# Kernel tuning notes

Measured on AMD Instinct MI355X. Metric: run time of the kernel, lower is better.

The kernel has to match this reference:

```python
import jax, jax.numpy as jnp
import numpy as np

DIM = 1024
HEADS = 16
DIM_HEAD = 64
INNER = HEADS * DIM_HEAD  # 1024
SCALE = DIM ** (-0.5)     # NOTE: source uses dim, not dim_head, for scaling


def setup_inputs() -> dict:
    key = jax.random.key(0)
    k_x, k_qkv, k_out = jax.random.split(key, 3)
    x = jax.random.normal(k_x, (4, 2048, DIM), dtype=jnp.float32)
    # store weights pre-transposed: y = x @ W  (equivalent to torch Linear with W.T)
    w_qkv = jax.random.normal(k_qkv, (DIM, 3 * INNER), dtype=jnp.float32) * 0.02
    w_out = jax.random.normal(k_out, (INNER, DIM), dtype=jnp.float32) * 0.02
    b_out = jnp.zeros((DIM,), dtype=jnp.float32)
    return {"x": x, "w_qkv": w_qkv, "w_out": w_out, "b_out": b_out}


def reference(x, w_qkv, w_out, b_out):
    b, n, _ = x.shape
    qkv = x @ w_qkv                                  # [b, n, 3*inner]
    q, k, v = jnp.split(qkv, 3, axis=-1)             # each [b, n, inner]

    def to_heads(t):
        return t.reshape(b, n, HEADS, DIM_HEAD).transpose(0, 2, 1, 3)  # [b, h, n, d]

    q, k, v = to_heads(q), to_heads(k), to_heads(v)
    dots = jnp.einsum("bhid,bhjd->bhij", q, k) * SCALE   # [b, h, n, n]
    attn = jax.nn.softmax(dots, axis=-1)
    out = jnp.einsum("bhij,bhjd->bhid", attn, v)         # [b, h, n, d]
    out = out.transpose(0, 2, 1, 3).reshape(b, n, INNER)  # [b, n, inner]
    return out @ w_out + b_out                            # dropout p=0 -> identity
```

## Files before the change

kernel.cpp:

```cpp
#include <hip/hip_runtime.h>
#include <math.h>

#define BATCH   4
#define NSEQ    2048
#define DIM     1024
#define HEADS   16
#define DHEAD   64
#define INNER   1024
#define MTOT    (BATCH*NSEQ)
#define SC_L2E  0.04508422f

typedef __attribute__((ext_vector_type(8))) unsigned short u16x8;
typedef __attribute__((ext_vector_type(4))) unsigned short u16x4;
typedef __attribute__((ext_vector_type(8))) short          bf16x8;
typedef __attribute__((ext_vector_type(4))) float          f32x4;

__device__ __forceinline__ unsigned short f2bf(float f) {
    unsigned int u = __builtin_bit_cast(unsigned int, f);
    u += 0x7FFFu + ((u >> 16) & 1u);
    return (unsigned short)(u >> 16);
}

__device__ __forceinline__ float fexp2(float x) {
    float r; asm("v_exp_f32 %0, %1" : "=v"(r) : "v"(x)); return r;
}

__device__ __forceinline__ unsigned int cvtpk(float lo, float hi) {
    unsigned int r; asm("v_cvt_pk_bf16_f32 %0, %1, %2" : "=v"(r) : "v"(lo), "v"(hi));
    return r;
}

#define GLDS16(gp, lp) __builtin_amdgcn_global_load_lds( \
    (const __attribute__((address_space(1))) unsigned int*)(gp), \
    (__attribute__((address_space(3))) unsigned int*)(lp), 16, 0, 0)

#define SWC(r, c) ((c) ^ (((r) & 7) << 3))

__global__ __launch_bounds__(256) void cvt_bf16(const float* __restrict__ in,
                                                unsigned short* __restrict__ out)
{
    const int i = blockIdx.x * 256 + threadIdx.x;
    const float4* p = reinterpret_cast<const float4*>(in) + (size_t)i * 2;
    float4 a = p[0], b = p[1];
    u16x8 o;
    o[0]=f2bf(a.x); o[1]=f2bf(a.y); o[2]=f2bf(a.z); o[3]=f2bf(a.w);
    o[4]=f2bf(b.x); o[5]=f2bf(b.y); o[6]=f2bf(b.z); o[7]=f2bf(b.w);
    reinterpret_cast<u16x8*>(out)[i] = o;
}

__global__ __launch_bounds__(256) void transp_bf16(const float* __restrict__ in,
                                                   unsigned short* __restrict__ out,
                                                   int R, int C)
{
    __shared__ float tile[32][33];
    const int c0 = blockIdx.x * 32, r0 = blockIdx.y * 32;
    const int tx = threadIdx.x & 31, ty = threadIdx.x >> 5;
#pragma unroll
    for (int i = 0; i < 32; i += 8)
        tile[ty + i][tx] = in[(size_t)(r0 + ty + i) * C + c0 + tx];
    __syncthreads();
#pragma unroll
    for (int i = 0; i < 32; i += 8)
        out[(size_t)(c0 + ty + i) * R + r0 + tx] = f2bf(tile[tx][ty + i]);
}


__global__ __launch_bounds__(256) void gemm_qkv_mfma(const unsigned short* __restrict__ A,
                                                     const unsigned short* __restrict__ Bt,
                                                     unsigned short* __restrict__ qb,
                                                     unsigned short* __restrict__ kb,
                                                     unsigned short* __restrict__ vt)
{
    __shared__ unsigned short As[128][32];
    __shared__ unsigned short Bs[128][32];

    const int t = threadIdx.x;
    const int l = t & 63, w = t >> 6;
    const int wr = w >> 1, wc = w & 1;
    const int g = l >> 4, ql = l & 15;

    const int lin  = blockIdx.x + 24 * blockIdx.y;
    const int nlin = (lin & 7) * 192 + (lin >> 3);
    const int bx = nlin % 24, by = nlin / 24;
    const int row0 = by * 128;
    const int col0 = bx * 128;
    const int lr = l >> 2, lc = l & 3;

    f32x4 acc[4][4];
#pragma unroll
    for (int mi = 0; mi < 4; ++mi)
#pragma unroll
        for (int ni = 0; ni < 4; ++ni)
#pragma unroll
            for (int r = 0; r < 4; ++r) acc[mi][ni][r] = 0.f;

    for (int k0 = 0; k0 < DIM; k0 += 32) {
        __syncthreads();
        {
            const unsigned short* ag = A  + (size_t)(row0 + 32 * w + lr) * DIM + k0 + lc * 8;
            const unsigned short* bg = Bt + (size_t)(col0 + 32 * w + lr) * DIM + k0 + lc * 8;
            GLDS16(ag,              &As[32 * w][0]);
            GLDS16(ag + 16 * DIM,   &As[32 * w + 16][0]);
            GLDS16(bg,              &Bs[32 * w][0]);
            GLDS16(bg + 16 * DIM,   &Bs[32 * w + 16][0]);
        }
        __syncthreads();

        bf16x8 af[4], bf[4];
#pragma unroll
        for (int mi = 0; mi < 4; ++mi)
            af[mi] = *reinterpret_cast<const bf16x8*>(&As[wr * 64 + mi * 16 + ql][g * 8]);
#pragma unroll
        for (int ni = 0; ni < 4; ++ni)
            bf[ni] = *reinterpret_cast<const bf16x8*>(&Bs[wc * 64 + ni * 16 + ql][g * 8]);
#pragma unroll
        for (int mi = 0; mi < 4; ++mi)
#pragma unroll
            for (int ni = 0; ni < 4; ++ni)
                acc[mi][ni] = __builtin_amdgcn_mfma_f32_16x16x32_bf16(af[mi], bf[ni], acc[mi][ni], 0, 0, 0);
    }

#pragma unroll
    for (int mi = 0; mi < 4; ++mi) {
        const int m0 = row0 + wr * 64 + mi * 16 + g * 4;
        const int b  = m0 >> 11, n0 = m0 & 2047;
#pragma unroll
        for (int ni = 0; ni < 4; ++ni) {
            const int c = col0 + wc * 64 + ni * 16 + ql;
            const int part = c >> 10, inner = c & 1023;
            const int h = inner >> 6, d = inner & 63;
            if (part == 2) {
                const int key0 = n0 & 63;
                const int nst  = (n0 & ~63)
                               | (key0 & 0x23)
                               | (((key0 >> 3) & 1) << 4)
                               | (((key0 >> 2) & 1) << 3)
                               | (((key0 >> 4) & 1) << 2);
                u16x4 pk;
#pragma unroll
                for (int r = 0; r < 4; ++r) pk[r] = f2bf(acc[mi][ni][r]);
                *reinterpret_cast<u16x4*>(&vt[(((size_t)b * HEADS + h) * DHEAD + d) * NSEQ + nst]) = pk;
            } else if (part == 0) {
                unsigned short* dst = qb + (((size_t)b * HEADS + h) * NSEQ + n0) * DHEAD + d;
#pragma unroll
                for (int r = 0; r < 4; ++r) dst[(size_t)r * DHEAD] = f2bf(acc[mi][ni][r] * SC_L2E);
            } else {
                unsigned short* dst = kb + (((size_t)b * HEADS + h) * NSEQ + n0) * DHEAD + d;
#pragma unroll
                for (int r = 0; r < 4; ++r) dst[(size_t)r * DHEAD] = f2bf(acc[mi][ni][r]);
            }
        }
    }
}

__global__ __launch_bounds__(256) void gemm_out_mfma(const unsigned short* __restrict__ A,
                                                     const unsigned short* __restrict__ Bt,
                                                     const float* __restrict__ bias,
                                                     float* __restrict__ out)
{
    __shared__ unsigned short As[128][32];
    __shared__ unsigned short Bs[128][32];

    const int t = threadIdx.x;
    const int l = t & 63, w = t >> 6;
    const int wr = w >> 1, wc = w & 1;
    const int g = l >> 4, ql = l & 15;

    const int lin  = blockIdx.x + 8 * blockIdx.y;
    const int nlin = (lin & 7) * 64 + (lin >> 3);
    const int bx = nlin % 8, by = nlin / 8;
    const int row0 = by * 128;
    const int col0 = bx * 128;
    const int lr = l >> 2, lc = l & 3;

    f32x4 acc[4][4];
#pragma unroll
    for (int mi = 0; mi < 4; ++mi)
#pragma unroll
        for (int ni = 0; ni < 4; ++ni)
#pragma unroll
            for (int r = 0; r < 4; ++r) acc[mi][ni][r] = 0.f;

    for (int k0 = 0; k0 < INNER; k0 += 32) {
        __syncthreads();
        {
            const unsigned short* ag = A  + (size_t)(row0 + 32 * w + lr) * INNER + k0 + lc * 8;
            const unsigned short* bg = Bt + (size_t)(col0 + 32 * w + lr) * INNER + k0 + lc * 8;
            GLDS16(ag,               &As[32 * w][0]);
            GLDS16(ag + 16 * INNER,  &As[32 * w + 16][0]);
            GLDS16(bg,               &Bs[32 * w][0]);
            GLDS16(bg + 16 * INNER,  &Bs[32 * w + 16][0]);
        }
        __syncthreads();

        bf16x8 af[4], bf[4];
#pragma unroll
        for (int mi = 0; mi < 4; ++mi)
            af[mi] = *reinterpret_cast<const bf16x8*>(&As[wr * 64 + mi * 16 + ql][g * 8]);
#pragma unroll
        for (int ni = 0; ni < 4; ++ni)
            bf[ni] = *reinterpret_cast<const bf16x8*>(&Bs[wc * 64 + ni * 16 + ql][g * 8]);
#pragma unroll
        for (int mi = 0; mi < 4; ++mi)
#pragma unroll
            for (int ni = 0; ni < 4; ++ni)
                acc[mi][ni] = __builtin_amdgcn_mfma_f32_16x16x32_bf16(af[mi], bf[ni], acc[mi][ni], 0, 0, 0);
    }

#pragma unroll
    for (int mi = 0; mi < 4; ++mi) {
        const int m0 = row0 + wr * 64 + mi * 16 + g * 4;
#pragma unroll
        for (int ni = 0; ni < 4; ++ni) {
            const int c = col0 + wc * 64 + ni * 16 + ql;
            const float bv = bias[c];
#pragma unroll
            for (int r = 0; r < 4; ++r)
                out[(size_t)(m0 + r) * DIM + c] = acc[mi][ni][r] + bv;
        }
    }
}

__global__ __launch_bounds__(512) void attn_mfma(const unsigned short* __restrict__ qg,
                                                 const unsigned short* __restrict__ kg,
                                                 const unsigned short* __restrict__ vtg,
                                                 unsigned short* __restrict__ og)
{
    __shared__ unsigned short Ks [2][64 * 64];
    __shared__ unsigned short Vts[2][64 * 64];

    const int bh = blockIdx.x;
    const int b = bh >> 4, h = bh & 15;
    const int qblk = blockIdx.y;
    const int t = threadIdx.x, l = t & 63, w = t >> 6;
    const int g = l >> 4, ql = l & 15;

    const size_t hb = (size_t)bh * NSEQ * DHEAD;

    bf16x8 qf[2][2];
#pragma unroll
    for (int qh = 0; qh < 2; ++qh) {
        const unsigned short* qrow = qg + hb + (size_t)(qblk * 256 + w * 32 + qh * 16 + ql) * DHEAD;
        qf[qh][0] = *reinterpret_cast<const bf16x8*>(qrow + g * 8);
        qf[qh][1] = *reinterpret_cast<const bf16x8*>(qrow + 32 + g * 8);
    }

    const int r = t >> 3, seg = t & 7;
    const unsigned short* kgp = kg  + hb + (size_t)r * DHEAD + seg * 8;
    const unsigned short* vgp = vtg + hb + (size_t)r * NSEQ  + seg * 8;
    const int st = r * 64 + ((seg ^ (r & 7)) * 8);

    {
        u16x8 k0 = *reinterpret_cast<const u16x8*>(kgp);
        u16x8 v0 = *reinterpret_cast<const u16x8*>(vgp);
        *reinterpret_cast<u16x8*>(&Ks [0][st]) = k0;
        *reinterpret_cast<u16x8*>(&Vts[0][st]) = v0;
    }
    __syncthreads();

    const unsigned short* kpre = kgp + 64 * DHEAD;
    const unsigned short* vpre = vgp + 64;

    f32x4 acc_o[2][4];
#pragma unroll
    for (int qh = 0; qh < 2; ++qh)
#pragma unroll
        for (int dt = 0; dt < 4; ++dt)
#pragma unroll
            for (int rr = 0; rr < 4; ++rr) acc_o[qh][dt][rr] = 0.f;
    float m_r[2] = {-INFINITY, -INFINITY};
    float l_r[2] = {0.f, 0.f};

    for (int kbi = 0; kbi < NSEQ / 64; ++kbi) {
        const int cur = kbi & 1;
        u16x8 nk, nv;
        const bool pre = (kbi + 1 < NSEQ / 64);
        if (pre) {
            nk = *reinterpret_cast<const u16x8*>(kpre);
            nv = *reinterpret_cast<const u16x8*>(vpre);
            kpre += 64 * DHEAD;
            vpre += 64;
        }

        f32x4 sacc[2][4];
#pragma unroll
        for (int qh = 0; qh < 2; ++qh)
#pragma unroll
            for (int jt = 0; jt < 4; ++jt)
#pragma unroll
                for (int rr = 0; rr < 4; ++rr) sacc[qh][jt][rr] = 0.f;
        __builtin_amdgcn_s_setprio(1);
#pragma unroll
        for (int jt = 0; jt < 4; ++jt) {
            const int row = jt * 16 + ql;
            bf16x8 kf0 = *reinterpret_cast<const bf16x8*>(&Ks[cur][row * 64 + SWC(row, g * 8)]);
            bf16x8 kf1 = *reinterpret_cast<const bf16x8*>(&Ks[cur][row * 64 + SWC(row, 32 + g * 8)]);
            sacc[0][jt] = __builtin_amdgcn_mfma_f32_16x16x32_bf16(kf0, qf[0][0], sacc[0][jt], 0, 0, 0);
            sacc[0][jt] = __builtin_amdgcn_mfma_f32_16x16x32_bf16(kf1, qf[0][1], sacc[0][jt], 0, 0, 0);
            sacc[1][jt] = __builtin_amdgcn_mfma_f32_16x16x32_bf16(kf0, qf[1][0], sacc[1][jt], 0, 0, 0);
            sacc[1][jt] = __builtin_amdgcn_mfma_f32_16x16x32_bf16(kf1, qf[1][1], sacc[1][jt], 0, 0, 0);
        }
        __builtin_amdgcn_s_setprio(0);

        bf16x8 pf[2][2];
#pragma unroll
        for (int qh = 0; qh < 2; ++qh) {
            float a0 = fmaxf(fmaxf(sacc[qh][0][0], sacc[qh][0][1]), sacc[qh][0][2]);
            float a1 = fmaxf(fmaxf(sacc[qh][0][3], sacc[qh][1][0]), sacc[qh][1][1]);
            float a2 = fmaxf(fmaxf(sacc[qh][1][2], sacc[qh][1][3]), sacc[qh][2][0]);
            float a3 = fmaxf(fmaxf(sacc[qh][2][1], sacc[qh][2][2]), sacc[qh][2][3]);
            float a4 = fmaxf(fmaxf(sacc[qh][3][0], sacc[qh][3][1]), sacc[qh][3][2]);
            float mx = fmaxf(fmaxf(fmaxf(a0, a1), a2), fmaxf(fmaxf(a3, a4), sacc[qh][3][3]));
            mx = fmaxf(mx, __shfl_xor(mx, 16));
            mx = fmaxf(mx, __shfl_xor(mx, 32));
            if (__any(mx > m_r[qh] + 8.f)) {
                const float m_new = fmaxf(m_r[qh], mx);
                const float alpha = fexp2(m_r[qh] - m_new);
                l_r[qh] *= alpha;
#pragma unroll
                for (int dt = 0; dt < 4; ++dt)
#pragma unroll
                    for (int rr = 0; rr < 4; ++rr) acc_o[qh][dt][rr] *= alpha;
                m_r[qh] = m_new;
            }
            float p[16];
#pragma unroll
            for (int jt = 0; jt < 4; ++jt)
#pragma unroll
                for (int rr = 0; rr < 4; ++rr)
                    p[jt * 4 + rr] = fexp2(sacc[qh][jt][rr] - m_r[qh]);
            float s0 = (p[0] + p[1]) + (p[2] + p[3]);
            float s1 = (p[4] + p[5]) + (p[6] + p[7]);
            float s2 = (p[8] + p[9]) + (p[10] + p[11]);
            float s3 = (p[12] + p[13]) + (p[14] + p[15]);
            float ps = (s0 + s1) + (s2 + s3);
            ps += __shfl_xor(ps, 16);
            ps += __shfl_xor(ps, 32);
            l_r[qh] += ps;

#pragma unroll
            for (int js = 0; js < 2; ++js) {
                unsigned int u0 = cvtpk(p[8 * js + 0], p[8 * js + 1]);
                unsigned int u1 = cvtpk(p[8 * js + 2], p[8 * js + 3]);
                unsigned int u2 = cvtpk(p[8 * js + 4], p[8 * js + 5]);
                unsigned int u3 = cvtpk(p[8 * js + 6], p[8 * js + 7]);
                uint4 uu = {u0, u1, u2, u3};
                pf[qh][js] = __builtin_bit_cast(bf16x8, uu);
            }
        }

        __builtin_amdgcn_s_setprio(1);
#pragma unroll
        for (int js = 0; js < 2; ++js) {
            bf16x8 vf[4];
#pragma unroll
            for (int dt = 0; dt < 4; ++dt) {
                const int row = dt * 16 + ql;
                vf[dt] = *reinterpret_cast<const bf16x8*>(&Vts[cur][row * 64 + SWC(row, js * 32 + g * 8)]);
            }
#pragma unroll
            for (int qh = 0; qh < 2; ++qh)
#pragma unroll
                for (int dt = 0; dt < 4; ++dt)
                    acc_o[qh][dt] = __builtin_amdgcn_mfma_f32_16x16x32_bf16(vf[dt], pf[qh][js], acc_o[qh][dt], 0, 0, 0);
        }
        __builtin_amdgcn_s_setprio(0);

        if (pre) {
            *reinterpret_cast<u16x8*>(&Ks [cur ^ 1][st]) = nk;
            *reinterpret_cast<u16x8*>(&Vts[cur ^ 1][st]) = nv;
        }
        __syncthreads();
    }

#pragma unroll
    for (int qh = 0; qh < 2; ++qh) {
        const float rinv = 1.0f / l_r[qh];
        const int n = qblk * 256 + w * 32 + qh * 16 + ql;
        unsigned short* dst = og + ((size_t)b * NSEQ + n) * INNER + h * DHEAD;
#pragma unroll
        for (int dt = 0; dt < 4; ++dt) {
            uint2 u;
            u.x = cvtpk(acc_o[qh][dt][0] * rinv, acc_o[qh][dt][1] * rinv);
            u.y = cvtpk(acc_o[qh][dt][2] * rinv, acc_o[qh][dt][3] * rinv);
            *reinterpret_cast<uint2*>(&dst[dt * 16 + g * 4]) = u;
        }
    }
}


extern "C" void kernel_launch(void* const* d_in, const int* in_sizes, int n_in,
                              void* d_out, int out_size, void* d_ws, size_t ws_size,
                              hipStream_t stream) {
    const float* x     = (const float*)d_in[0];
    const float* w_qkv = (const float*)d_in[1];
    const float* w_out = (const float*)d_in[2];
    const float* b_out = (const float*)d_in[3];
    float* out = (float*)d_out;

    unsigned short* ws = (unsigned short*)d_ws;
    const size_t nX  = (size_t)MTOT * DIM;
    const size_t nWq = (size_t)DIM * 3 * INNER;
    const size_t nWo = (size_t)DIM * INNER;
    unsigned short* Xb  = ws;
    unsigned short* Wqt = Xb  + nX;
    unsigned short* Wot = Wqt + nWq;
    unsigned short* qb  = Wot + nWo;
    unsigned short* kb  = qb  + nX;
    unsigned short* vt  = kb  + nX;
    unsigned short* Ob  = vt  + nX;

    cvt_bf16<<<dim3(nX / 8 / 256), dim3(256), 0, stream>>>(x, Xb);
    transp_bf16<<<dim3(3 * INNER / 32, DIM / 32), dim3(256), 0, stream>>>(w_qkv, Wqt, DIM, 3 * INNER);
    transp_bf16<<<dim3(DIM / 32, INNER / 32), dim3(256), 0, stream>>>(w_out, Wot, INNER, DIM);

    gemm_qkv_mfma<<<dim3(3 * INNER / 128, MTOT / 128), dim3(256), 0, stream>>>(Xb, Wqt, qb, kb, vt);
    attn_mfma<<<dim3(BATCH * HEADS, NSEQ / 256), dim3(512), 0, stream>>>(qb, kb, vt, Ob);
    gemm_out_mfma<<<dim3(DIM / 128, MTOT / 128), dim3(256), 0, stream>>>(Ob, Wot, b_out, out);
}
```

Measured before the change: 199.0 us.

## Fuse prep kernels and stream K/V tiles into LDS via global_load_lds

The three preprocessing launches (x conversion and two weight transposes) become one kernel that dispatches on block index, which removes two launches and their gaps. In the attention kernel, K and V^T tiles are now loaded directly into LDS with global_load_lds DMA, using a source-side XOR swizzle, instead of staging through registers. The prefetch of the next tile is issued at the top of the iteration and written straight into the other buffer. This frees registers and overlaps the loads with the MFMA work, but relies on the swizzle mapping and the barrier to keep the loaded data correct.

```diff
diff --git a/kernel.cpp b/kernel.cpp
--- a/kernel.cpp
+++ b/kernel.cpp
@@ -36,24 +36,36 @@
 
 #define SWC(r, c) ((c) ^ (((r) & 7) << 3))
 
-__global__ __launch_bounds__(256) void cvt_bf16(const float* __restrict__ in,
-                                                unsigned short* __restrict__ out)
-{
-    const int i = blockIdx.x * 256 + threadIdx.x;
-    const float4* p = reinterpret_cast<const float4*>(in) + (size_t)i * 2;
-    float4 a = p[0], b = p[1];
-    u16x8 o;
-    o[0]=f2bf(a.x); o[1]=f2bf(a.y); o[2]=f2bf(a.z); o[3]=f2bf(a.w);
-    o[4]=f2bf(b.x); o[5]=f2bf(b.y); o[6]=f2bf(b.z); o[7]=f2bf(b.w);
-    reinterpret_cast<u16x8*>(out)[i] = o;
-}
-
-__global__ __launch_bounds__(256) void transp_bf16(const float* __restrict__ in,
-                                                   unsigned short* __restrict__ out,
-                                                   int R, int C)
+__global__ __launch_bounds__(256) void prep_fused(const float* __restrict__ x,
+                                                  const float* __restrict__ w_qkv,
+                                                  const float* __restrict__ w_out,
+                                                  unsigned short* __restrict__ Xb,
+                                                  unsigned short* __restrict__ Wqt,
+                                                  unsigned short* __restrict__ Wot)
 {
     __shared__ float tile[32][33];
-    const int c0 = blockIdx.x * 32, r0 = blockIdx.y * 32;
+    const int bid = blockIdx.x;
+    if (bid < 4096) {
+        const int i = bid * 256 + threadIdx.x;
+        const float4* p = reinterpret_cast<const float4*>(x) + (size_t)i * 2;
+        float4 a = p[0], b = p[1];
+        u16x8 o;
+        o[0]=f2bf(a.x); o[1]=f2bf(a.y); o[2]=f2bf(a.z); o[3]=f2bf(a.w);
+        o[4]=f2bf(b.x); o[5]=f2bf(b.y); o[6]=f2bf(b.z); o[7]=f2bf(b.w);
+        reinterpret_cast<u16x8*>(Xb)[i] = o;
+        return;
+    }
+    const float* in; unsigned short* out; int R, C, bx, by;
+    if (bid < 4096 + 3072) {
+        const int lin = bid - 4096;
+        in = w_qkv; out = Wqt; R = DIM; C = 3 * INNER;
+        bx = lin % 96; by = lin / 96;
+    } else {
+        const int lin = bid - (4096 + 3072);
+        in = w_out; out = Wot; R = INNER; C = DIM;
+        bx = lin & 31; by = lin >> 5;
+    }
+    const int c0 = bx * 32, r0 = by * 32;
     const int tx = threadIdx.x & 31, ty = threadIdx.x >> 5;
 #pragma unroll
     for (int i = 0; i < 32; i += 8)
@@ -245,21 +257,14 @@
         qf[qh][1] = *reinterpret_cast<const bf16x8*>(qrow + 32 + g * 8);
     }
 
-    const int r = t >> 3, seg = t & 7;
-    const unsigned short* kgp = kg  + hb + (size_t)r * DHEAD + seg * 8;
-    const unsigned short* vgp = vtg + hb + (size_t)r * NSEQ  + seg * 8;
-    const int st = r * 64 + ((seg ^ (r & 7)) * 8);
-
-    {
-        u16x8 k0 = *reinterpret_cast<const u16x8*>(kgp);
-        u16x8 v0 = *reinterpret_cast<const u16x8*>(vgp);
-        *reinterpret_cast<u16x8*>(&Ks [0][st]) = k0;
-        *reinterpret_cast<u16x8*>(&Vts[0][st]) = v0;
-    }
+    const int srow  = l >> 3;
+    const int sslot = (l & 7) ^ srow;
+    const unsigned short* kSrc = kg  + hb + (size_t)(w * 8 + srow) * DHEAD + sslot * 8;
+    const unsigned short* vSrc = vtg + hb + (size_t)(w * 8 + srow) * NSEQ  + sslot * 8;
+
+    GLDS16(kSrc, &Ks [0][(w * 8) * 64]);
+    GLDS16(vSrc, &Vts[0][(w * 8) * 64]);
     __syncthreads();
-
-    const unsigned short* kpre = kgp + 64 * DHEAD;
-    const unsigned short* vpre = vgp + 64;
 
     f32x4 acc_o[2][4];
 #pragma unroll
@@ -273,13 +278,9 @@
 
     for (int kbi = 0; kbi < NSEQ / 64; ++kbi) {
         const int cur = kbi & 1;
-        u16x8 nk, nv;
-        const bool pre = (kbi + 1 < NSEQ / 64);
-        if (pre) {
-            nk = *reinterpret_cast<const u16x8*>(kpre);
-            nv = *reinterpret_cast<const u16x8*>(vpre);
-            kpre += 64 * DHEAD;
-            vpre += 64;
+        if (kbi + 1 < NSEQ / 64) {
+            GLDS16(kSrc + (size_t)(kbi + 1) * 64 * DHEAD, &Ks [cur ^ 1][(w * 8) * 64]);
+            GLDS16(vSrc + (size_t)(kbi + 1) * 64,         &Vts[cur ^ 1][(w * 8) * 64]);
         }
 
         f32x4 sacc[2][4];
@@ -366,10 +367,6 @@
         }
         __builtin_amdgcn_s_setprio(0);
 
-        if (pre) {
-            *reinterpret_cast<u16x8*>(&Ks [cur ^ 1][st]) = nk;
-            *reinterpret_cast<u16x8*>(&Vts[cur ^ 1][st]) = nv;
-        }
         __syncthreads();
     }
 
@@ -410,10 +407,7 @@
     unsigned short* vt  = kb  + nX;
     unsigned short* Ob  = vt  + nX;
 
-    cvt_bf16<<<dim3(nX / 8 / 256), dim3(256), 0, stream>>>(x, Xb);
-    transp_bf16<<<dim3(3 * INNER / 32, DIM / 32), dim3(256), 0, stream>>>(w_qkv, Wqt, DIM, 3 * INNER);
-    transp_bf16<<<dim3(DIM / 32, INNER / 32), dim3(256), 0, stream>>>(w_out, Wot, INNER, DIM);
-
+    prep_fused<<<dim3(4096 + 3072 + 1024), dim3(256), 0, stream>>>(x, w_qkv, w_out, Xb, Wqt, Wot);
     gemm_qkv_mfma<<<dim3(3 * INNER / 128, MTOT / 128), dim3(256), 0, stream>>>(Xb, Wqt, qb, kb, vt);
     attn_mfma<<<dim3(BATCH * HEADS, NSEQ / 256), dim3(512), 0, stream>>>(qb, kb, vt, Ob);
     gemm_out_mfma<<<dim3(DIM / 128, MTOT / 128), dim3(256), 0, stream>>>(Ob, Wot, b_out, out);
```

Result: no change. 196.8 us (-1.1%).
